# Kernel optimization log

Measured on AMD Instinct MI355X. Metric: run time of the kernel, lower is better.

Reference implementation:

```python
import jax, jax.numpy as jnp
import numpy as np

M = 10          # modules per layer (args.M)
IN_DIM = 784    # 28*28
H = 20          # module width
NUM_CLASSES = 10
BATCH = 65536


def setup_inputs() -> dict:
    key = jax.random.key(0)
    ks = jax.random.split(key, 10)
    s1 = 1.0 / np.sqrt(IN_DIM)
    s2 = 1.0 / np.sqrt(H)
    return {
        "x": jax.random.normal(ks[0], (BATCH, IN_DIM), dtype=jnp.float32),
        "W1": jax.random.uniform(ks[1], (M, H, IN_DIM), jnp.float32, -s1, s1),
        "b1": jax.random.uniform(ks[2], (M, H), jnp.float32, -s1, s1),
        "W2": jax.random.uniform(ks[3], (M, H, H), jnp.float32, -s2, s2),
        "b2": jax.random.uniform(ks[4], (M, H), jnp.float32, -s2, s2),
        "W3": jax.random.uniform(ks[5], (M, H, H), jnp.float32, -s2, s2),
        "b3": jax.random.uniform(ks[6], (M, H), jnp.float32, -s2, s2),
        "Wl": jax.random.uniform(ks[7], (NUM_CLASSES, H), jnp.float32, -s2, s2),
        "bl": jax.random.uniform(ks[8], (NUM_CLASSES,), jnp.float32, -s2, s2),
        "pathway": jax.random.randint(ks[9], (3, 3), 0, M, dtype=jnp.int64),
    }


def _active(row):
    # Faithful to torch: list(set(pathway[l])) then sum_layer keeps only
    # the first element (len==1) or the sum of the first two elements.
    # CPython set of small ints iterates in sorted order.
    uniq = sorted(set(int(v) for v in np.asarray(row)))
    return np.asarray(uniq[:2], dtype=np.int64)


def _expert_layer(h, W, b, idx):
    # h: [B, F]; W[idx]: [k, H, F]; relu per module, then sum over the <=2 kept modules
    out = jax.nn.relu(jnp.einsum('bf,kof->kbo', h, W[idx]) + b[idx][:, None, :])
    return out.sum(axis=0)


def reference(x, W1, b1, W2, b2, W3, b3, Wl, bl, pathway):
    pw = np.asarray(pathway)  # pathway is static routing metadata
    i1, i2, i3 = _active(pw[0]), _active(pw[1]), _active(pw[2])
    h1 = _expert_layer(x, W1, b1, i1)    # [B, 20]
    h2 = _expert_layer(h1, W2, b2, i2)   # [B, 20]
    h3 = _expert_layer(h2, W3, b3, i3)   # [B, 20]
    return h3 @ Wl.T + bl                # [B, 10]
```

## Files before the change

### kernel.cpp

```cpp
#include <hip/hip_runtime.h>

#define BATCH   65536
#define IN_DIM  784
#define HDIM    20
#define NCLS    10
#define THREADS 256
#define SPW     16
#define SPB     64
#define NFULL   24
#define NWROWS  48

#define OFF_WHC  0
#define OFF_W2C  76800
#define OFF_W3C  79872
#define OFF_WLC  82944
#define OFF_BC   83968
#define OFF_BLC  84544

#define ABUF(b)  (smem + (size_t)(b) * 8192)
#define BBUF(b)  (smem + 32768 + (size_t)(b) * 3072)
#define WAITVM(N) asm volatile("s_waitcnt vmcnt(" #N ")" ::: "memory")

typedef __attribute__((ext_vector_type(2))) __fp16   fp16x2;
typedef __attribute__((ext_vector_type(8))) _Float16 f16x8;
typedef __attribute__((ext_vector_type(4))) float    f32x4;
typedef __attribute__((ext_vector_type(4))) unsigned u32x4;

typedef union { uint4 q; f16x8 v; } BFrag;
typedef union { fp16x2 h[4]; f16x8 v; } AFrag;
typedef union { fp16x2 h[2]; uint2 u; } Pack4;
typedef union { u32x4 u; float f[4]; } AU;
typedef union { u32x4 u; f16x8 v; } BU;

__device__ __forceinline__ void gld16(const void* g, void* l) {
    __builtin_amdgcn_global_load_lds(
        (const __attribute__((address_space(1))) unsigned int*)g,
        (__attribute__((address_space(3))) unsigned int*)l, 16, 0, 0);
}

__device__ __forceinline__ void route(const int* pw, bool is64, int row,
                                      int& e0, int& e1, float& m) {
    int v0, v1, v2;
    if (is64) {
        v0 = pw[(row * 3 + 0) * 2];
        v1 = pw[(row * 3 + 1) * 2];
        v2 = pw[(row * 3 + 2) * 2];
    } else {
        v0 = pw[row * 3 + 0];
        v1 = pw[row * 3 + 1];
        v2 = pw[row * 3 + 2];
    }
    int lo  = min(v0, min(v1, v2));
    int hi  = max(v0, max(v1, v2));
    int mid = v0 + v1 + v2 - lo - hi;
    e0 = lo;
    if (mid != lo)     { e1 = mid; m = 1.0f; }
    else if (hi != lo) { e1 = hi;  m = 1.0f; }
    else               { e1 = lo;  m = 0.0f; }
}

__global__ __launch_bounds__(256)
void cvt_all_kernel(const float* __restrict__ W1, const float* __restrict__ W2,
                    const float* __restrict__ W3, const float* __restrict__ Wl,
                    const float* __restrict__ b1, const float* __restrict__ b2,
                    const float* __restrict__ b3, const float* __restrict__ bl,
                    const int* __restrict__ pathway, char* __restrict__ ws) {
    const int gid = blockIdx.x * 256 + threadIdx.x;

    bool is64 = ((pathway[1] | pathway[3] | pathway[5] | pathway[7]) == 0);
    int e10, e11, e20, e21, e30, e31;
    float m1, m2, m3;
    route(pathway, is64, 0, e10, e11, m1);
    route(pathway, is64, 1, e20, e21, m2);
    route(pathway, is64, 2, e30, e31, m3);

    if (gid < NWROWS * (IN_DIM / 8)) {
        const int u  = gid / (IN_DIM / 8);
        const int k8 = gid % (IN_DIM / 8);
        uint4 outw = make_uint4(0, 0, 0, 0);
        if (u < 2 * HDIM) {
            const int e = (u < HDIM) ? e10 : e11;
            const int o = (u < HDIM) ? u : u - HDIM;
            const float* src = W1 + ((size_t)e * HDIM + o) * IN_DIM + k8 * 8;
            const float4 v0 = *reinterpret_cast<const float4*>(src);
            const float4 v1 = *reinterpret_cast<const float4*>(src + 4);
            Pack4 p0, p1;
            p0.h[0] = __builtin_amdgcn_cvt_pkrtz(v0.x, v0.y);
            p0.h[1] = __builtin_amdgcn_cvt_pkrtz(v0.z, v0.w);
            p1.h[0] = __builtin_amdgcn_cvt_pkrtz(v1.x, v1.y);
            p1.h[1] = __builtin_amdgcn_cvt_pkrtz(v1.z, v1.w);
            outw = make_uint4(p0.u.x, p0.u.y, p1.u.x, p1.u.y);
        }
        *reinterpret_cast<uint4*>((_Float16*)(ws + OFF_WHC) + (size_t)u * IN_DIM + k8 * 8) = outw;
        return;
    }

    const int g2 = gid - NWROWS * (IN_DIM / 8);
    if (g2 < 1536) {
        const int u = g2 >> 5, k = g2 & 31;
        float v = 0.0f;
        if (u < 2 * HDIM && k < HDIM) {
            const int e = (u < HDIM) ? e20 : e21;
            const int o = (u < HDIM) ? u : u - HDIM;
            v = W2[((size_t)e * HDIM + o) * HDIM + k];
        }
        ((_Float16*)(ws + OFF_W2C))[g2] = (_Float16)v;
    } else if (g2 < 3072) {
        const int i = g2 - 1536;
        const int u = i >> 5, k = i & 31;
        float v = 0.0f;
        if (u < 2 * HDIM && k < HDIM) {
            const int e = (u < HDIM) ? e30 : e31;
            const int o = (u < HDIM) ? u : u - HDIM;
            v = W3[((size_t)e * HDIM + o) * HDIM + k];
        }
        ((_Float16*)(ws + OFF_W3C))[i] = (_Float16)v;
    } else if (g2 < 3584) {
        const int i = g2 - 3072;
        const int c = i >> 5, k = i & 31;
        float v = (c < NCLS && k < HDIM) ? Wl[c * HDIM + k] : 0.0f;
        ((_Float16*)(ws + OFF_WLC))[i] = (_Float16)v;
    } else if (g2 < 3728) {
        const int i = g2 - 3584;
        const int l = i / 48, hb = (i % 48) / 24, c = i % 24;
        float v = 0.0f;
        if (c < HDIM) {
            int e;
            const float* B;
            if (l == 0)      { e = hb ? e11 : e10; B = b1; }
            else if (l == 1) { e = hb ? e21 : e20; B = b2; }
            else             { e = hb ? e31 : e30; B = b3; }
            v = B[e * HDIM + c];
        }
        ((float*)(ws + OFF_BC))[i] = v;
    } else if (g2 < 3744) {
        const int c = g2 - 3728;
        ((float*)(ws + OFF_BLC))[c] = (c < NCLS) ? bl[c] : 0.0f;
    }
}

__device__ __forceinline__ void stageA(char* smem, int buf, int kstep,
                                       const float* __restrict__ xg,
                                       int w, int lane) {
#pragma unroll
    for (int j = 0; j < 2; ++j) {
        const int q    = w * 2 + j;
        const int row  = q * 8 + (lane >> 3);
        const int c    = (lane & 7) ^ (lane >> 3);
        const float* g = xg + (size_t)row * IN_DIM + kstep * 32 + c * 4;
        gld16(g, ABUF(buf) + q * 1024);
    }
}

__device__ __forceinline__ void stageB(char* smem, int buf, int kstep,
                                       const _Float16* __restrict__ Whc,
                                       int w, int lane) {
    if (w < 3) {
        const int row = w * 16 + (lane >> 2);
        const int c   = (lane & 3) ^ ((lane >> 3) & 3);
        const _Float16* g = Whc + (size_t)row * IN_DIM + kstep * 32 + c * 8;
        gld16(g, BBUF(buf) + w * 1024);
    }
}

__device__ __forceinline__ void computeAsm(int a0a, int a1a, int b0a, int b1a,
                                           int b2a, f32x4 acc[3]) {
    u32x4 a0, a1, b0, b1, b2;
    asm volatile("ds_read_b128 %0, %1" : "=v"(a0) : "v"(a0a));
    asm volatile("ds_read_b128 %0, %1" : "=v"(a1) : "v"(a1a));
    asm volatile("ds_read_b128 %0, %1" : "=v"(b0) : "v"(b0a));
    asm volatile("ds_read_b128 %0, %1" : "=v"(b1) : "v"(b1a));
    asm volatile("ds_read_b128 %0, %1" : "=v"(b2) : "v"(b2a));
    asm volatile("s_waitcnt lgkmcnt(0)" ::: "memory");
    __builtin_amdgcn_sched_barrier(0);
    AU ua0, ua1;
    ua0.u = a0; ua1.u = a1;
    AFrag af;
    af.h[0] = __builtin_amdgcn_cvt_pkrtz(ua0.f[0], ua0.f[1]);
    af.h[1] = __builtin_amdgcn_cvt_pkrtz(ua0.f[2], ua0.f[3]);
    af.h[2] = __builtin_amdgcn_cvt_pkrtz(ua1.f[0], ua1.f[1]);
    af.h[3] = __builtin_amdgcn_cvt_pkrtz(ua1.f[2], ua1.f[3]);
    BU ub0, ub1, ub2;
    ub0.u = b0; ub1.u = b1; ub2.u = b2;
    acc[0] = __builtin_amdgcn_mfma_f32_16x16x32_f16(af.v, ub0.v, acc[0], 0, 0, 0);
    acc[1] = __builtin_amdgcn_mfma_f32_16x16x32_f16(af.v, ub1.v, acc[1], 0, 0, 0);
    acc[2] = __builtin_amdgcn_mfma_f32_16x16x32_f16(af.v, ub2.v, acc[2], 0, 0, 0);
}

__global__ __launch_bounds__(THREADS)
void pathnet_kernel(const float* __restrict__ x, const char* __restrict__ ws,
                    const int* __restrict__ pathway, float* __restrict__ out)
{
    __shared__ __align__(16) char smem[45056];

    const int t    = threadIdx.x;
    const int lane = t & 63;
    const int w    = __builtin_amdgcn_readfirstlane(t >> 6);
    const bool wlt3 = (w < 3);

    bool is64 = ((pathway[1] | pathway[3] | pathway[5] | pathway[7]) == 0);
    int e10, e11, e20, e21, e30, e31;
    float m1, m2, m3;
    route(pathway, is64, 0, e10, e11, m1);
    route(pathway, is64, 1, e20, e21, m2);
    route(pathway, is64, 2, e30, e31, m3);

    const _Float16* Whc = (const _Float16*)(ws + OFF_WHC);
    const int sbase0 = blockIdx.x * SPB;
    const float* xg = x + (size_t)sbase0 * IN_DIM;

    const int row16 = lane & 15;
    const int kg    = lane >> 4;
    const int arow  = w * 16 + row16;
    const int aoff0 = arow * 128 + (((2 * kg + 0) ^ (arow & 7)) * 16);
    const int aoff1 = arow * 128 + (((2 * kg + 1) ^ (arow & 7)) * 16);
    int boff[3];
#pragma unroll
    for (int tt = 0; tt < 3; ++tt) {
        const int u = tt * 16 + row16;
        boff[tt] = 32768 + u * 64 + ((kg ^ ((u >> 1) & 3)) * 16);
    }

    f32x4 acc[3];
#pragma unroll
    for (int tt = 0; tt < 3; ++tt) acc[tt] = (f32x4){0.f, 0.f, 0.f, 0.f};

    stageA(smem, 0, 0, xg, w, lane);  stageB(smem, 0, 0, Whc, w, lane);
    stageA(smem, 1, 1, xg, w, lane);  stageB(smem, 1, 1, Whc, w, lane);

#pragma unroll
    for (int i = 0; i < NFULL; ++i) {
        if (i + 2 < NFULL) {
            stageA(smem, (i + 2) & 3, i + 2, xg, w, lane);
            stageB(smem, (i + 2) & 3, i + 2, Whc, w, lane);
        }
        if (i < NFULL - 2)       { if (wlt3) WAITVM(6); else WAITVM(4); }
        else if (i == NFULL - 2) { if (wlt3) WAITVM(3); else WAITVM(2); }
        else                     { WAITVM(0); }
        __builtin_amdgcn_s_barrier();
        asm volatile("" ::: "memory");
        const int bb = (i & 3);
        computeAsm(aoff0 + bb * 8192, aoff1 + bb * 8192,
                   boff[0] + bb * 3072, boff[1] + bb * 3072, boff[2] + bb * 3072,
                   acc);
    }

    {
        AFrag af;
        BFrag bf[3];
        if (kg < 2) {
            const float* ap = xg + (size_t)(w * 16 + row16) * IN_DIM + 768 + kg * 8;
            const float4 q0 = *reinterpret_cast<const float4*>(ap);
            const float4 q1 = *reinterpret_cast<const float4*>(ap + 4);
            af.h[0] = __builtin_amdgcn_cvt_pkrtz(q0.x, q0.y);
            af.h[1] = __builtin_amdgcn_cvt_pkrtz(q0.z, q0.w);
            af.h[2] = __builtin_amdgcn_cvt_pkrtz(q1.x, q1.y);
            af.h[3] = __builtin_amdgcn_cvt_pkrtz(q1.z, q1.w);
#pragma unroll
            for (int tt = 0; tt < 3; ++tt) {
                const int u = tt * 16 + row16;
                bf[tt].q = *reinterpret_cast<const uint4*>(Whc + (size_t)u * IN_DIM + 768 + kg * 8);
            }
        } else {
            const fp16x2 z = __builtin_amdgcn_cvt_pkrtz(0.f, 0.f);
            af.h[0] = af.h[1] = af.h[2] = af.h[3] = z;
#pragma unroll
            for (int tt = 0; tt < 3; ++tt) bf[tt].q = make_uint4(0, 0, 0, 0);
        }
#pragma unroll
        for (int tt = 0; tt < 3; ++tt)
            acc[tt] = __builtin_amdgcn_mfma_f32_16x16x32_f16(af.v, bf[tt].v, acc[tt], 0, 0, 0);
    }

    float* pre = reinterpret_cast<float*>(smem) + w * (16 * 44);

#pragma unroll
    for (int tt = 0; tt < 3; ++tt) {
        const int col = tt * 16 + row16;
        if (col < 2 * HDIM) {
#pragma unroll
            for (int r = 0; r < 4; ++r)
                pre[(kg * 4 + r) * 44 + col] = acc[tt][r];
        }
    }

    const _Float16* W2c = (const _Float16*)(ws + OFF_W2C);
    const _Float16* W3c = (const _Float16*)(ws + OFF_W3C);
    const _Float16* Wlc = (const _Float16*)(ws + OFF_WLC);
    const float*    bc  = (const float*)(ws + OFF_BC);
    const float*    blc = (const float*)(ws + OFF_BLC);

    BFrag w2f[3], w3f[3], wlf;
#pragma unroll
    for (int tt = 0; tt < 3; ++tt) {
        const int u = tt * 16 + row16;
        w2f[tt].q = *reinterpret_cast<const uint4*>(W2c + u * 32 + kg * 8);
        w3f[tt].q = *reinterpret_cast<const uint4*>(W3c + u * 32 + kg * 8);
    }
    wlf.q = *reinterpret_cast<const uint4*>(Wlc + row16 * 32 + kg * 8);
    const float blv = blc[row16];

    const float* prow = pre + row16 * 44;

    auto buildA = [&](const float* b0, const float* b1, float mm) -> AFrag {
        AFrag af;
        if (kg == 3) {
            const fp16x2 z = __builtin_amdgcn_cvt_pkrtz(0.f, 0.f);
            af.h[0] = af.h[1] = af.h[2] = af.h[3] = z;
            return af;
        }
        const float* p = prow + kg * 8;
        const float4 p0 = *reinterpret_cast<const float4*>(p);
        const float4 p1 = *reinterpret_cast<const float4*>(p + 4);
        const float4 q0 = *reinterpret_cast<const float4*>(p + 20);
        const float4 q1 = *reinterpret_cast<const float4*>(p + 24);
        const float4 c0 = *reinterpret_cast<const float4*>(b0 + kg * 8);
        const float4 c1 = *reinterpret_cast<const float4*>(b0 + kg * 8 + 4);
        const float4 d0 = *reinterpret_cast<const float4*>(b1 + kg * 8);
        const float4 d1 = *reinterpret_cast<const float4*>(b1 + kg * 8 + 4);
        float h[8];
        h[0] = fmaxf(p0.x + c0.x, 0.f) + mm * fmaxf(q0.x + d0.x, 0.f);
        h[1] = fmaxf(p0.y + c0.y, 0.f) + mm * fmaxf(q0.y + d0.y, 0.f);
        h[2] = fmaxf(p0.z + c0.z, 0.f) + mm * fmaxf(q0.z + d0.z, 0.f);
        h[3] = fmaxf(p0.w + c0.w, 0.f) + mm * fmaxf(q0.w + d0.w, 0.f);
        h[4] = fmaxf(p1.x + c1.x, 0.f) + mm * fmaxf(q1.x + d1.x, 0.f);
        h[5] = fmaxf(p1.y + c1.y, 0.f) + mm * fmaxf(q1.y + d1.y, 0.f);
        h[6] = fmaxf(p1.z + c1.z, 0.f) + mm * fmaxf(q1.z + d1.z, 0.f);
        h[7] = fmaxf(p1.w + c1.w, 0.f) + mm * fmaxf(q1.w + d1.w, 0.f);
        if (kg == 2) { h[4] = h[5] = h[6] = h[7] = 0.f; }
        af.h[0] = __builtin_amdgcn_cvt_pkrtz(h[0], h[1]);
        af.h[1] = __builtin_amdgcn_cvt_pkrtz(h[2], h[3]);
        af.h[2] = __builtin_amdgcn_cvt_pkrtz(h[4], h[5]);
        af.h[3] = __builtin_amdgcn_cvt_pkrtz(h[6], h[7]);
        return af;
    };

    AFrag a1 = buildA(bc + 0, bc + 24, m1);
    f32x4 acc2[3];
#pragma unroll
    for (int tt = 0; tt < 3; ++tt) {
        acc2[tt] = (f32x4){0.f, 0.f, 0.f, 0.f};
        acc2[tt] = __builtin_amdgcn_mfma_f32_16x16x32_f16(a1.v, w2f[tt].v, acc2[tt], 0, 0, 0);
    }
#pragma unroll
    for (int tt = 0; tt < 3; ++tt) {
        const int col = tt * 16 + row16;
        if (col < 2 * HDIM) {
#pragma unroll
            for (int r = 0; r < 4; ++r)
                pre[(kg * 4 + r) * 44 + col] = acc2[tt][r];
        }
    }

    AFrag a2 = buildA(bc + 48, bc + 72, m2);
    f32x4 acc3[3];
#pragma unroll
    for (int tt = 0; tt < 3; ++tt) {
        acc3[tt] = (f32x4){0.f, 0.f, 0.f, 0.f};
        acc3[tt] = __builtin_amdgcn_mfma_f32_16x16x32_f16(a2.v, w3f[tt].v, acc3[tt], 0, 0, 0);
    }
#pragma unroll
    for (int tt = 0; tt < 3; ++tt) {
        const int col = tt * 16 + row16;
        if (col < 2 * HDIM) {
#pragma unroll
            for (int r = 0; r < 4; ++r)
                pre[(kg * 4 + r) * 44 + col] = acc3[tt][r];
        }
    }

    AFrag a3 = buildA(bc + 96, bc + 120, m3);
    f32x4 accY = (f32x4){0.f, 0.f, 0.f, 0.f};
    accY = __builtin_amdgcn_mfma_f32_16x16x32_f16(a3.v, wlf.v, accY, 0, 0, 0);

    if (row16 < NCLS) {
#pragma unroll
        for (int r = 0; r < 4; ++r) {
            const int srow = sbase0 + w * SPW + kg * 4 + r;
            out[(size_t)srow * NCLS + row16] = accY[r] + blv;
        }
    }
}

extern "C" void kernel_launch(void* const* d_in, const int* in_sizes, int n_in,
                              void* d_out, int out_size, void* d_ws, size_t ws_size,
                              hipStream_t stream) {
    const float* x  = (const float*)d_in[0];
    const float* W1 = (const float*)d_in[1];
    const float* b1 = (const float*)d_in[2];
    const float* W2 = (const float*)d_in[3];
    const float* b2 = (const float*)d_in[4];
    const float* W3 = (const float*)d_in[5];
    const float* b3 = (const float*)d_in[6];
    const float* Wl = (const float*)d_in[7];
    const float* bl = (const float*)d_in[8];
    const int*   pw = (const int*)d_in[9];
    float* out = (float*)d_out;
    char* ws = (char*)d_ws;

    const int ntask = NWROWS * (IN_DIM / 8) + 3744;
    cvt_all_kernel<<<(ntask + 255) / 256, 256, 0, stream>>>(
        W1, W2, W3, Wl, b1, b2, b3, bl, pw, ws);

    dim3 grid(BATCH / SPB);
    pathnet_kernel<<<grid, THREADS, 0, stream>>>(x, ws, pw, out);
}
```

Baseline: 42.34 us.

## Drop weight-conversion pre-kernel; stream fp32 W1 rows directly via routed pointers

Removes the separate kernel that gathered the routed expert weights into fp16 in a workspace. The main kernel now computes routed row pointers itself and streams fp32 W1 tiles into shared memory on a 3-deep buffer. Each tile is converted to fp16 in registers before the MFMA. W2, W3, Wl and the biases are read straight from the original fp32 tensors. This saves a kernel launch and the workspace round trip, but doubles W1 bytes per block and adds conversion instructions and shared-memory reads in the inner loop.

```diff
diff --git a/kernel.cpp b/kernel.cpp
--- a/kernel.cpp
+++ b/kernel.cpp
@@ -8,17 +8,9 @@
 #define SPW     16
 #define SPB     64
 #define NFULL   24
-#define NWROWS  48
-
-#define OFF_WHC  0
-#define OFF_W2C  76800
-#define OFF_W3C  79872
-#define OFF_WLC  82944
-#define OFF_BC   83968
-#define OFF_BLC  84544
 
 #define ABUF(b)  (smem + (size_t)(b) * 8192)
-#define BBUF(b)  (smem + 32768 + (size_t)(b) * 3072)
+#define BBUF(b)  (smem + 32768 + (size_t)(b) * 6144)
 #define WAITVM(N) asm volatile("s_waitcnt vmcnt(" #N ")" ::: "memory")
 
 typedef __attribute__((ext_vector_type(2))) __fp16   fp16x2;
@@ -26,16 +18,17 @@
 typedef __attribute__((ext_vector_type(4))) float    f32x4;
 typedef __attribute__((ext_vector_type(4))) unsigned u32x4;
 
-typedef union { uint4 q; f16x8 v; } BFrag;
-typedef union { fp16x2 h[4]; f16x8 v; } AFrag;
-typedef union { fp16x2 h[2]; uint2 u; } Pack4;
-typedef union { u32x4 u; float f[4]; } AU;
-typedef union { u32x4 u; f16x8 v; } BU;
+typedef union { fp16x2 h[4]; f16x8 v; } Frag;
+typedef union { u32x4 u; float f[4]; } FU;
 
 __device__ __forceinline__ void gld16(const void* g, void* l) {
     __builtin_amdgcn_global_load_lds(
         (const __attribute__((address_space(1))) unsigned int*)g,
         (__attribute__((address_space(3))) unsigned int*)l, 16, 0, 0);
+}
+
+__device__ __forceinline__ fp16x2 cvt2(float a, float b) {
+    return __builtin_amdgcn_cvt_pkrtz(a, b);
 }
 
 __device__ __forceinline__ void route(const int* pw, bool is64, int row,
@@ -59,13 +52,49 @@
     else               { e1 = lo;  m = 0.0f; }
 }
 
-__global__ __launch_bounds__(256)
-void cvt_all_kernel(const float* __restrict__ W1, const float* __restrict__ W2,
-                    const float* __restrict__ W3, const float* __restrict__ Wl,
-                    const float* __restrict__ b1, const float* __restrict__ b2,
-                    const float* __restrict__ b3, const float* __restrict__ bl,
-                    const int* __restrict__ pathway, char* __restrict__ ws) {
-    const int gid = blockIdx.x * 256 + threadIdx.x;
+__device__ __forceinline__ const float* urow(const float* W, int u,
+                                             int eLo, int eHi, int rowlen) {
+    int e, o;
+    if (u < HDIM)          { e = eLo; o = u; }
+    else if (u < 2 * HDIM) { e = eHi; o = u - HDIM; }
+    else                   { e = eLo; o = 0; }
+    return W + (size_t)(e * HDIM + o) * rowlen;
+}
+
+__device__ __forceinline__ void stageA(char* smem, int buf, int kstep,
+                                       const float* __restrict__ xg,
+                                       int w, int lane) {
+#pragma unroll
+    for (int j = 0; j < 2; ++j) {
+        const int q    = w * 2 + j;
+        const int row  = q * 8 + (lane >> 3);
+        const int c    = (lane & 7) ^ (lane >> 3);
+        const float* g = xg + (size_t)row * IN_DIM + kstep * 32 + c * 4;
+        gld16(g, ABUF(buf) + q * 1024);
+    }
+}
+
+__device__ __forceinline__ void stageB(char* smem, int buf, int kstep,
+                                       const float* bq0, const float* bq1,
+                                       int q0, int nq) {
+    gld16(bq0 + kstep * 32, BBUF(buf) + q0 * 1024);
+    if (nq == 2) gld16(bq1 + kstep * 32, BBUF(buf) + (q0 + 1) * 1024);
+}
+
+__global__ __launch_bounds__(THREADS)
+void pathnet_kernel(const float* __restrict__ x,
+                    const float* __restrict__ W1, const float* __restrict__ b1,
+                    const float* __restrict__ W2, const float* __restrict__ b2,
+                    const float* __restrict__ W3, const float* __restrict__ b3,
+                    const float* __restrict__ Wl, const float* __restrict__ bl,
+                    const int*   __restrict__ pathway, float* __restrict__ out)
+{
+    __shared__ __align__(16) char smem[51200];
+
+    const int t    = threadIdx.x;
+    const int lane = t & 63;
+    const int w    = __builtin_amdgcn_readfirstlane(t >> 6);
+    const bool wlt2 = (w < 2);
 
     bool is64 = ((pathway[1] | pathway[3] | pathway[5] | pathway[7]) == 0);
     int e10, e11, e20, e21, e30, e31;
@@ -74,198 +103,106 @@
     route(pathway, is64, 1, e20, e21, m2);
     route(pathway, is64, 2, e30, e31, m3);
 
-    if (gid < NWROWS * (IN_DIM / 8)) {
-        const int u  = gid / (IN_DIM / 8);
-        const int k8 = gid % (IN_DIM / 8);
-        uint4 outw = make_uint4(0, 0, 0, 0);
-        if (u < 2 * HDIM) {
-            const int e = (u < HDIM) ? e10 : e11;
-            const int o = (u < HDIM) ? u : u - HDIM;
-            const float* src = W1 + ((size_t)e * HDIM + o) * IN_DIM + k8 * 8;
-            const float4 v0 = *reinterpret_cast<const float4*>(src);
-            const float4 v1 = *reinterpret_cast<const float4*>(src + 4);
-            Pack4 p0, p1;
-            p0.h[0] = __builtin_amdgcn_cvt_pkrtz(v0.x, v0.y);
-            p0.h[1] = __builtin_amdgcn_cvt_pkrtz(v0.z, v0.w);
-            p1.h[0] = __builtin_amdgcn_cvt_pkrtz(v1.x, v1.y);
-            p1.h[1] = __builtin_amdgcn_cvt_pkrtz(v1.z, v1.w);
-            outw = make_uint4(p0.u.x, p0.u.y, p1.u.x, p1.u.y);
-        }
-        *reinterpret_cast<uint4*>((_Float16*)(ws + OFF_WHC) + (size_t)u * IN_DIM + k8 * 8) = outw;
-        return;
-    }
-
-    const int g2 = gid - NWROWS * (IN_DIM / 8);
-    if (g2 < 1536) {
-        const int u = g2 >> 5, k = g2 & 31;
-        float v = 0.0f;
-        if (u < 2 * HDIM && k < HDIM) {
-            const int e = (u < HDIM) ? e20 : e21;
-            const int o = (u < HDIM) ? u : u - HDIM;
-            v = W2[((size_t)e * HDIM + o) * HDIM + k];
-        }
-        ((_Float16*)(ws + OFF_W2C))[g2] = (_Float16)v;
-    } else if (g2 < 3072) {
-        const int i = g2 - 1536;
-        const int u = i >> 5, k = i & 31;
-        float v = 0.0f;
-        if (u < 2 * HDIM && k < HDIM) {
-            const int e = (u < HDIM) ? e30 : e31;
-            const int o = (u < HDIM) ? u : u - HDIM;
-            v = W3[((size_t)e * HDIM + o) * HDIM + k];
-        }
-        ((_Float16*)(ws + OFF_W3C))[i] = (_Float16)v;
-    } else if (g2 < 3584) {
-        const int i = g2 - 3072;
-        const int c = i >> 5, k = i & 31;
-        float v = (c < NCLS && k < HDIM) ? Wl[c * HDIM + k] : 0.0f;
-        ((_Float16*)(ws + OFF_WLC))[i] = (_Float16)v;
-    } else if (g2 < 3728) {
-        const int i = g2 - 3584;
-        const int l = i / 48, hb = (i % 48) / 24, c = i % 24;
-        float v = 0.0f;
-        if (c < HDIM) {
-            int e;
-            const float* B;
-            if (l == 0)      { e = hb ? e11 : e10; B = b1; }
-            else if (l == 1) { e = hb ? e21 : e20; B = b2; }
-            else             { e = hb ? e31 : e30; B = b3; }
-            v = B[e * HDIM + c];
-        }
-        ((float*)(ws + OFF_BC))[i] = v;
-    } else if (g2 < 3744) {
-        const int c = g2 - 3728;
-        ((float*)(ws + OFF_BLC))[c] = (c < NCLS) ? bl[c] : 0.0f;
-    }
-}
-
-__device__ __forceinline__ void stageA(char* smem, int buf, int kstep,
-                                       const float* __restrict__ xg,
-                                       int w, int lane) {
-#pragma unroll
-    for (int j = 0; j < 2; ++j) {
-        const int q    = w * 2 + j;
-        const int row  = q * 8 + (lane >> 3);
-        const int c    = (lane & 7) ^ (lane >> 3);
-        const float* g = xg + (size_t)row * IN_DIM + kstep * 32 + c * 4;
-        gld16(g, ABUF(buf) + q * 1024);
-    }
-}
-
-__device__ __forceinline__ void stageB(char* smem, int buf, int kstep,
-                                       const _Float16* __restrict__ Whc,
-                                       int w, int lane) {
-    if (w < 3) {
-        const int row = w * 16 + (lane >> 2);
-        const int c   = (lane & 3) ^ ((lane >> 3) & 3);
-        const _Float16* g = Whc + (size_t)row * IN_DIM + kstep * 32 + c * 8;
-        gld16(g, BBUF(buf) + w * 1024);
-    }
-}
-
-__device__ __forceinline__ void computeAsm(int a0a, int a1a, int b0a, int b1a,
-                                           int b2a, f32x4 acc[3]) {
-    u32x4 a0, a1, b0, b1, b2;
-    asm volatile("ds_read_b128 %0, %1" : "=v"(a0) : "v"(a0a));
-    asm volatile("ds_read_b128 %0, %1" : "=v"(a1) : "v"(a1a));
-    asm volatile("ds_read_b128 %0, %1" : "=v"(b0) : "v"(b0a));
-    asm volatile("ds_read_b128 %0, %1" : "=v"(b1) : "v"(b1a));
-    asm volatile("ds_read_b128 %0, %1" : "=v"(b2) : "v"(b2a));
-    asm volatile("s_waitcnt lgkmcnt(0)" ::: "memory");
-    __builtin_amdgcn_sched_barrier(0);
-    AU ua0, ua1;
-    ua0.u = a0; ua1.u = a1;
-    AFrag af;
-    af.h[0] = __builtin_amdgcn_cvt_pkrtz(ua0.f[0], ua0.f[1]);
-    af.h[1] = __builtin_amdgcn_cvt_pkrtz(ua0.f[2], ua0.f[3]);
-    af.h[2] = __builtin_amdgcn_cvt_pkrtz(ua1.f[0], ua1.f[1]);
-    af.h[3] = __builtin_amdgcn_cvt_pkrtz(ua1.f[2], ua1.f[3]);
-    BU ub0, ub1, ub2;
-    ub0.u = b0; ub1.u = b1; ub2.u = b2;
-    acc[0] = __builtin_amdgcn_mfma_f32_16x16x32_f16(af.v, ub0.v, acc[0], 0, 0, 0);
-    acc[1] = __builtin_amdgcn_mfma_f32_16x16x32_f16(af.v, ub1.v, acc[1], 0, 0, 0);
-    acc[2] = __builtin_amdgcn_mfma_f32_16x16x32_f16(af.v, ub2.v, acc[2], 0, 0, 0);
-}
-
-__global__ __launch_bounds__(THREADS)
-void pathnet_kernel(const float* __restrict__ x, const char* __restrict__ ws,
-                    const int* __restrict__ pathway, float* __restrict__ out)
-{
-    __shared__ __align__(16) char smem[45056];
-
-    const int t    = threadIdx.x;
-    const int lane = t & 63;
-    const int w    = __builtin_amdgcn_readfirstlane(t >> 6);
-    const bool wlt3 = (w < 3);
-
-    bool is64 = ((pathway[1] | pathway[3] | pathway[5] | pathway[7]) == 0);
-    int e10, e11, e20, e21, e30, e31;
-    float m1, m2, m3;
-    route(pathway, is64, 0, e10, e11, m1);
-    route(pathway, is64, 1, e20, e21, m2);
-    route(pathway, is64, 2, e30, e31, m3);
-
-    const _Float16* Whc = (const _Float16*)(ws + OFF_WHC);
     const int sbase0 = blockIdx.x * SPB;
     const float* xg = x + (size_t)sbase0 * IN_DIM;
+
+    const int q0  = wlt2 ? (w * 2) : (w + 2);
+    const int nq  = wlt2 ? 2 : 1;
+    const int brow0 = q0 * 8 + (lane >> 3);
+    const int brow1 = (q0 + 1) * 8 + (lane >> 3);
+    const int bcsw  = ((lane & 7) ^ (lane >> 3)) * 4;
+    const float* bq0 = urow(W1, brow0, e10, e11, IN_DIM) + bcsw;
+    const float* bq1 = urow(W1, brow1, e10, e11, IN_DIM) + bcsw;
 
     const int row16 = lane & 15;
     const int kg    = lane >> 4;
     const int arow  = w * 16 + row16;
     const int aoff0 = arow * 128 + (((2 * kg + 0) ^ (arow & 7)) * 16);
     const int aoff1 = arow * 128 + (((2 * kg + 1) ^ (arow & 7)) * 16);
-    int boff[3];
+    int boffL[3], boffH[3];
 #pragma unroll
     for (int tt = 0; tt < 3; ++tt) {
         const int u = tt * 16 + row16;
-        boff[tt] = 32768 + u * 64 + ((kg ^ ((u >> 1) & 3)) * 16);
+        boffL[tt] = 32768 + u * 128 + (((2 * kg + 0) ^ (u & 7)) * 16);
+        boffH[tt] = 32768 + u * 128 + (((2 * kg + 1) ^ (u & 7)) * 16);
     }
 
     f32x4 acc[3];
 #pragma unroll
     for (int tt = 0; tt < 3; ++tt) acc[tt] = (f32x4){0.f, 0.f, 0.f, 0.f};
 
-    stageA(smem, 0, 0, xg, w, lane);  stageB(smem, 0, 0, Whc, w, lane);
-    stageA(smem, 1, 1, xg, w, lane);  stageB(smem, 1, 1, Whc, w, lane);
+    stageB(smem, 0, 0, bq0, bq1, q0, nq);
+    stageA(smem, 0, 0, xg, w, lane);
+    stageA(smem, 1, 1, xg, w, lane);
 
 #pragma unroll
     for (int i = 0; i < NFULL; ++i) {
-        if (i + 2 < NFULL) {
-            stageA(smem, (i + 2) & 3, i + 2, xg, w, lane);
-            stageB(smem, (i + 2) & 3, i + 2, Whc, w, lane);
-        }
-        if (i < NFULL - 2)       { if (wlt3) WAITVM(6); else WAITVM(4); }
-        else if (i == NFULL - 2) { if (wlt3) WAITVM(3); else WAITVM(2); }
+        if (i + 1 < NFULL) stageB(smem, (i + 1) % 3, i + 1, bq0, bq1, q0, nq);
+        if (i + 2 < NFULL) stageA(smem, (i + 2) & 3, i + 2, xg, w, lane);
+        if (i < NFULL - 2)       { if (wlt2) WAITVM(6); else WAITVM(5); }
+        else if (i == NFULL - 2) { if (wlt2) WAITVM(4); else WAITVM(3); }
         else                     { WAITVM(0); }
         __builtin_amdgcn_s_barrier();
         asm volatile("" ::: "memory");
-        const int bb = (i & 3);
-        computeAsm(aoff0 + bb * 8192, aoff1 + bb * 8192,
-                   boff[0] + bb * 3072, boff[1] + bb * 3072, boff[2] + bb * 3072,
-                   acc);
+
+        const int bbA = (i & 3) * 8192;
+        const int bbB = (i % 3) * 6144;
+        u32x4 a0, a1, p0, p1, r0, r1, s0, s1;
+        asm volatile("ds_read_b128 %0, %1" : "=v"(a0) : "v"(aoff0 + bbA));
+        asm volatile("ds_read_b128 %0, %1" : "=v"(a1) : "v"(aoff1 + bbA));
+        asm volatile("ds_read_b128 %0, %1" : "=v"(p0) : "v"(boffL[0] + bbB));
+        asm volatile("ds_read_b128 %0, %1" : "=v"(p1) : "v"(boffH[0] + bbB));
+        asm volatile("ds_read_b128 %0, %1" : "=v"(r0) : "v"(boffL[1] + bbB));
+        asm volatile("ds_read_b128 %0, %1" : "=v"(r1) : "v"(boffH[1] + bbB));
+        asm volatile("ds_read_b128 %0, %1" : "=v"(s0) : "v"(boffL[2] + bbB));
+        asm volatile("ds_read_b128 %0, %1" : "=v"(s1) : "v"(boffH[2] + bbB));
+        asm volatile("s_waitcnt lgkmcnt(0)" ::: "memory");
+        __builtin_amdgcn_sched_barrier(0);
+
+        FU ua0, ua1;
+        ua0.u = a0; ua1.u = a1;
+        Frag af;
+        af.h[0] = cvt2(ua0.f[0], ua0.f[1]); af.h[1] = cvt2(ua0.f[2], ua0.f[3]);
+        af.h[2] = cvt2(ua1.f[0], ua1.f[1]); af.h[3] = cvt2(ua1.f[2], ua1.f[3]);
+        FU v0, v1;
+        Frag bf;
+        v0.u = p0; v1.u = p1;
+        bf.h[0] = cvt2(v0.f[0], v0.f[1]); bf.h[1] = cvt2(v0.f[2], v0.f[3]);
+        bf.h[2] = cvt2(v1.f[0], v1.f[1]); bf.h[3] = cvt2(v1.f[2], v1.f[3]);
+        acc[0] = __builtin_amdgcn_mfma_f32_16x16x32_f16(af.v, bf.v, acc[0], 0, 0, 0);
+        v0.u = r0; v1.u = r1;
+        bf.h[0] = cvt2(v0.f[0], v0.f[1]); bf.h[1] = cvt2(v0.f[2], v0.f[3]);
+        bf.h[2] = cvt2(v1.f[0], v1.f[1]); bf.h[3] = cvt2(v1.f[2], v1.f[3]);
+        acc[1] = __builtin_amdgcn_mfma_f32_16x16x32_f16(af.v, bf.v, acc[1], 0, 0, 0);
+        v0.u = s0; v1.u = s1;
+        bf.h[0] = cvt2(v0.f[0], v0.f[1]); bf.h[1] = cvt2(v0.f[2], v0.f[3]);
+        bf.h[2] = cvt2(v1.f[0], v1.f[1]); bf.h[3] = cvt2(v1.f[2], v1.f[3]);
+        acc[2] = __builtin_amdgcn_mfma_f32_16x16x32_f16(af.v, bf.v, acc[2], 0, 0, 0);
     }
 
     {
-        AFrag af;
-        BFrag bf[3];
+        const fp16x2 z = cvt2(0.f, 0.f);
+        Frag af;
+        Frag bf[3];
         if (kg < 2) {
             const float* ap = xg + (size_t)(w * 16 + row16) * IN_DIM + 768 + kg * 8;
-            const float4 q0 = *reinterpret_cast<const float4*>(ap);
-            const float4 q1 = *reinterpret_cast<const float4*>(ap + 4);
-            af.h[0] = __builtin_amdgcn_cvt_pkrtz(q0.x, q0.y);
-            af.h[1] = __builtin_amdgcn_cvt_pkrtz(q0.z, q0.w);
-            af.h[2] = __builtin_amdgcn_cvt_pkrtz(q1.x, q1.y);
-            af.h[3] = __builtin_amdgcn_cvt_pkrtz(q1.z, q1.w);
+            const float4 a4 = *reinterpret_cast<const float4*>(ap);
+            const float4 a5 = *reinterpret_cast<const float4*>(ap + 4);
+            af.h[0] = cvt2(a4.x, a4.y); af.h[1] = cvt2(a4.z, a4.w);
+            af.h[2] = cvt2(a5.x, a5.y); af.h[3] = cvt2(a5.z, a5.w);
 #pragma unroll
             for (int tt = 0; tt < 3; ++tt) {
-                const int u = tt * 16 + row16;
-                bf[tt].q = *reinterpret_cast<const uint4*>(Whc + (size_t)u * IN_DIM + 768 + kg * 8);
+                const float* bp = urow(W1, tt * 16 + row16, e10, e11, IN_DIM) + 768 + kg * 8;
+                const float4 b4 = *reinterpret_cast<const float4*>(bp);
+                const float4 b5 = *reinterpret_cast<const float4*>(bp + 4);
+                bf[tt].h[0] = cvt2(b4.x, b4.y); bf[tt].h[1] = cvt2(b4.z, b4.w);
+                bf[tt].h[2] = cvt2(b5.x, b5.y); bf[tt].h[3] = cvt2(b5.z, b5.w);
             }
         } else {
-            const fp16x2 z = __builtin_amdgcn_cvt_pkrtz(0.f, 0.f);
             af.h[0] = af.h[1] = af.h[2] = af.h[3] = z;
 #pragma unroll
-            for (int tt = 0; tt < 3; ++tt) bf[tt].q = make_uint4(0, 0, 0, 0);
+            for (int tt = 0; tt < 3; ++tt)
+                bf[tt].h[0] = bf[tt].h[1] = bf[tt].h[2] = bf[tt].h[3] = z;
         }
 #pragma unroll
         for (int tt = 0; tt < 3; ++tt)
@@ -284,28 +221,56 @@
         }
     }
 
-    const _Float16* W2c = (const _Float16*)(ws + OFF_W2C);
-    const _Float16* W3c = (const _Float16*)(ws + OFF_W3C);
-    const _Float16* Wlc = (const _Float16*)(ws + OFF_WLC);
-    const float*    bc  = (const float*)(ws + OFF_BC);
-    const float*    blc = (const float*)(ws + OFF_BLC);
-
-    BFrag w2f[3], w3f[3], wlf;
+    const fp16x2 z = cvt2(0.f, 0.f);
+
+    auto loadRow8 = [&](const float* base) -> Frag {
+        Frag f;
+        if (kg < 2) {
+            const float4 lo = *reinterpret_cast<const float4*>(base + kg * 8);
+            const float4 hi = *reinterpret_cast<const float4*>(base + kg * 8 + 4);
+            f.h[0] = cvt2(lo.x, lo.y); f.h[1] = cvt2(lo.z, lo.w);
+            f.h[2] = cvt2(hi.x, hi.y); f.h[3] = cvt2(hi.z, hi.w);
+        } else if (kg == 2) {
+            const float4 lo = *reinterpret_cast<const float4*>(base + 16);
+            f.h[0] = cvt2(lo.x, lo.y); f.h[1] = cvt2(lo.z, lo.w);
+            f.h[2] = z; f.h[3] = z;
+        } else {
+            f.h[0] = f.h[1] = f.h[2] = f.h[3] = z;
+        }
+        return f;
+    };
+
+    Frag w2f[3], w3f[3], wlf;
 #pragma unroll
     for (int tt = 0; tt < 3; ++tt) {
         const int u = tt * 16 + row16;
-        w2f[tt].q = *reinterpret_cast<const uint4*>(W2c + u * 32 + kg * 8);
-        w3f[tt].q = *reinterpret_cast<const uint4*>(W3c + u * 32 + kg * 8);
-    }
-    wlf.q = *reinterpret_cast<const uint4*>(Wlc + row16 * 32 + kg * 8);
-    const float blv = blc[row16];
+        w2f[tt] = loadRow8(urow(W2, u, e20, e21, HDIM));
+        w3f[tt] = loadRow8(urow(W3, u, e30, e31, HDIM));
+    }
+    wlf = loadRow8(Wl + (size_t)((row16 < NCLS) ? row16 : 0) * HDIM);
+    const float blv = (row16 < NCLS) ? bl[row16] : 0.f;
 
     const float* prow = pre + row16 * 44;
 
-    auto buildA = [&](const float* b0, const float* b1, float mm) -> AFrag {
-        AFrag af;
+    auto loadBias8 = [&](const float* B, int e, float o8[8]) {
+        const float* base = B + e * HDIM;
+        if (kg < 2) {
+            const float4 lo = *reinterpret_cast<const float4*>(base + kg * 8);
+            const float4 hi = *reinterpret_cast<const float4*>(base + kg * 8 + 4);
+            o8[0] = lo.x; o8[1] = lo.y; o8[2] = lo.z; o8[3] = lo.w;
+            o8[4] = hi.x; o8[5] = hi.y; o8[6] = hi.z; o8[7] = hi.w;
+        } else if (kg == 2) {
+            const float4 lo = *reinterpret_cast<const float4*>(base + 16);
+            o8[0] = lo.x; o8[1] = lo.y; o8[2] = lo.z; o8[3] = lo.w;
+            o8[4] = o8[5] = o8[6] = o8[7] = 0.f;
+        } else {
+            for (int j = 0; j < 8; ++j) o8[j] = 0.f;
+        }
+    };
+
+    auto buildA = [&](const float* B, int eLo, int eHi, float mm) -> Frag {
+        Frag af;
         if (kg == 3) {
-            const fp16x2 z = __builtin_amdgcn_cvt_pkrtz(0.f, 0.f);
             af.h[0] = af.h[1] = af.h[2] = af.h[3] = z;
             return af;
         }
@@ -314,28 +279,25 @@
         const float4 p1 = *reinterpret_cast<const float4*>(p + 4);
         const float4 q0 = *reinterpret_cast<const float4*>(p + 20);
         const float4 q1 = *reinterpret_cast<const float4*>(p + 24);
-        const float4 c0 = *reinterpret_cast<const float4*>(b0 + kg * 8);
-        const float4 c1 = *reinterpret_cast<const float4*>(b0 + kg * 8 + 4);
-        const float4 d0 = *reinterpret_cast<const float4*>(b1 + kg * 8);
-        const float4 d1 = *reinterpret_cast<const float4*>(b1 + kg * 8 + 4);
+        float c8[8], d8[8];
+        loadBias8(B, eLo, c8);
+        loadBias8(B, eHi, d8);
         float h[8];
-        h[0] = fmaxf(p0.x + c0.x, 0.f) + mm * fmaxf(q0.x + d0.x, 0.f);
-        h[1] = fmaxf(p0.y + c0.y, 0.f) + mm * fmaxf(q0.y + d0.y, 0.f);
-        h[2] = fmaxf(p0.z + c0.z, 0.f) + mm * fmaxf(q0.z + d0.z, 0.f);
-        h[3] = fmaxf(p0.w + c0.w, 0.f) + mm * fmaxf(q0.w + d0.w, 0.f);
-        h[4] = fmaxf(p1.x + c1.x, 0.f) + mm * fmaxf(q1.x + d1.x, 0.f);
-        h[5] = fmaxf(p1.y + c1.y, 0.f) + mm * fmaxf(q1.y + d1.y, 0.f);
-        h[6] = fmaxf(p1.z + c1.z, 0.f) + mm * fmaxf(q1.z + d1.z, 0.f);
-        h[7] = fmaxf(p1.w + c1.w, 0.f) + mm * fmaxf(q1.w + d1.w, 0.f);
+        h[0] = fmaxf(p0.x + c8[0], 0.f) + mm * fmaxf(q0.x + d8[0], 0.f);
+        h[1] = fmaxf(p0.y + c8[1], 0.f) + mm * fmaxf(q0.y + d8[1], 0.f);
+        h[2] = fmaxf(p0.z + c8[2], 0.f) + mm * fmaxf(q0.z + d8[2], 0.f);
+        h[3] = fmaxf(p0.w + c8[3], 0.f) + mm * fmaxf(q0.w + d8[3], 0.f);
+        h[4] = fmaxf(p1.x + c8[4], 0.f) + mm * fmaxf(q1.x + d8[4], 0.f);
+        h[5] = fmaxf(p1.y + c8[5], 0.f) + mm * fmaxf(q1.y + d8[5], 0.f);
+        h[6] = fmaxf(p1.z + c8[6], 0.f) + mm * fmaxf(q1.z + d8[6], 0.f);
+        h[7] = fmaxf(p1.w + c8[7], 0.f) + mm * fmaxf(q1.w + d8[7], 0.f);
         if (kg == 2) { h[4] = h[5] = h[6] = h[7] = 0.f; }
-        af.h[0] = __builtin_amdgcn_cvt_pkrtz(h[0], h[1]);
-        af.h[1] = __builtin_amdgcn_cvt_pkrtz(h[2], h[3]);
-        af.h[2] = __builtin_amdgcn_cvt_pkrtz(h[4], h[5]);
-        af.h[3] = __builtin_amdgcn_cvt_pkrtz(h[6], h[7]);
+        af.h[0] = cvt2(h[0], h[1]); af.h[1] = cvt2(h[2], h[3]);
+        af.h[2] = cvt2(h[4], h[5]); af.h[3] = cvt2(h[6], h[7]);
         return af;
     };
 
-    AFrag a1 = buildA(bc + 0, bc + 24, m1);
+    Frag a1 = buildA(b1, e10, e11, m1);
     f32x4 acc2[3];
 #pragma unroll
     for (int tt = 0; tt < 3; ++tt) {
@@ -352,7 +314,7 @@
         }
     }
 
-    AFrag a2 = buildA(bc + 48, bc + 72, m2);
+    Frag a2 = buildA(b2, e20, e21, m2);
     f32x4 acc3[3];
 #pragma unroll
     for (int tt = 0; tt < 3; ++tt) {
@@ -369,7 +331,7 @@
         }
     }
 
-    AFrag a3 = buildA(bc + 96, bc + 120, m3);
+    Frag a3 = buildA(b3, e30, e31, m3);
     f32x4 accY = (f32x4){0.f, 0.f, 0.f, 0.f};
     accY = __builtin_amdgcn_mfma_f32_16x16x32_f16(a3.v, wlf.v, accY, 0, 0, 0);
 
@@ -396,12 +358,8 @@
     const float* bl = (const float*)d_in[8];
     const int*   pw = (const int*)d_in[9];
     float* out = (float*)d_out;
-    char* ws = (char*)d_ws;
-
-    const int ntask = NWROWS * (IN_DIM / 8) + 3744;
-    cvt_all_kernel<<<(ntask + 255) / 256, 256, 0, stream>>>(
-        W1, W2, W3, Wl, b1, b2, b3, bl, pw, ws);
 
     dim3 grid(BATCH / SPB);
-    pathnet_kernel<<<grid, THREADS, 0, stream>>>(x, ws, pw, out);
-}
+    pathnet_kernel<<<grid, THREADS, 0, stream>>>(x, W1, b1, W2, b2,
+                                                 W3, b3, Wl, bl, pw, out);
+}
```

Result: slower. 49.48 us (+16.9%).
